# Kernel tuning notes

Hardware: AMD Instinct MI355X
Metric: run time of the kernel (lower is better)

Reference implementation:

```python
import jax, jax.numpy as jnp
import numpy as np

N_NODES = 10000
N_EDGES = 160000
IN_F = 512
H_F = 512
OUT_F = 512


def _graph_conv(x, W, b, src, dst, norm_out, norm_in):
    # DGL GraphConv, norm='both': out = D_in^{-1/2} A D_out^{-1/2} X W + b
    xs = x * norm_out[:, None]            # scale src features by out-deg^-1/2
    msgs = xs[src]                        # gather: [E, F]
    agg = jax.ops.segment_sum(msgs, dst, num_segments=N_NODES)  # scatter-sum
    agg = agg * norm_in[:, None]          # scale by in-deg^-1/2
    return agg @ W + b


def setup_inputs() -> dict:
    key = jax.random.key(0)
    ks = jax.random.split(key, 10)
    inputs = jax.random.normal(ks[0], (N_NODES, IN_F), dtype=jnp.float32)
    src = jax.random.randint(ks[1], (N_EDGES,), 0, N_NODES, dtype=jnp.int32)
    dst = jax.random.randint(ks[2], (N_EDGES,), 0, N_NODES, dtype=jnp.int32)
    # Glorot-ish init for GraphConv weights, zero bias (DGL default)
    def glorot(k, fan_in, fan_out):
        s = jnp.sqrt(6.0 / (fan_in + fan_out)).astype(jnp.float32)
        return jax.random.uniform(k, (fan_in, fan_out), jnp.float32, -s, s)
    W1 = glorot(ks[3], IN_F, H_F)
    b1 = jnp.zeros((H_F,), jnp.float32)
    W2 = glorot(ks[4], H_F, H_F)
    b2 = jnp.zeros((H_F,), jnp.float32)
    W3 = glorot(ks[5], H_F, OUT_F)
    b3 = jnp.zeros((OUT_F,), jnp.float32)
    return {"inputs": inputs, "W1": W1, "b1": b1, "W2": W2, "b2": b2,
            "W3": W3, "b3": b3, "src": src, "dst": dst}


def reference(inputs, W1, b1, W2, b2, W3, b3, src, dst):
    ones = jnp.ones((N_EDGES,), jnp.float32)
    deg_out = jax.ops.segment_sum(ones, src, num_segments=N_NODES)
    deg_in = jax.ops.segment_sum(ones, dst, num_segments=N_NODES)
    norm_out = jnp.where(deg_out > 0, deg_out ** -0.5, 0.0)
    norm_in = jnp.where(deg_in > 0, deg_in ** -0.5, 0.0)

    h1 = jax.nn.relu(_graph_conv(inputs, W1, b1, src, dst, norm_out, norm_in))
    h2 = jax.nn.relu(_graph_conv(h1, W2, b2, src, dst, norm_out, norm_in))
    # NOTE: original module applies gcn_layer_2 a second time here (not layer 3)
    h3 = jax.nn.relu(_graph_conv(h2, W2, b2, src, dst, norm_out, norm_in))
    h4 = _graph_conv(h2, W3, b3, src, dst, norm_out, norm_in)
    return (h4, h3, h2)
```

## Files before the change

kernel.cpp:

```cpp
#include <hip/hip_runtime.h>

#define N_NODES 10000
#define N_EDGES 160000
#define FEAT 512
#define M_PAD 10048
#define QSTRIDE 1286144

typedef unsigned int uint32;

typedef __attribute__((ext_vector_type(8))) _Float16 half8;
typedef __attribute__((ext_vector_type(4))) float f32x4;


__device__ __forceinline__ void load_lds16(const void* g, void* l) {
    __builtin_amdgcn_global_load_lds(
        (const __attribute__((address_space(1))) void*)g,
        (__attribute__((address_space(3))) void*)l, 16, 0, 0);
}

__global__ void deg_kernel(const int* __restrict__ src, const int* __restrict__ dst,
                           int* __restrict__ deg_out, int* __restrict__ deg_in) {
    int e = blockIdx.x * blockDim.x + threadIdx.x;
    if (e < N_EDGES) {
        atomicAdd(&deg_out[src[e]], 1);
        atomicAdd(&deg_in[dst[e]], 1);
    }
}

__global__ void norm_kernel(const int* __restrict__ deg_out, const int* __restrict__ deg_in,
                            float* __restrict__ norm_out, float* __restrict__ norm_in) {
    int i = blockIdx.x * blockDim.x + threadIdx.x;
    if (i < N_NODES) {
        int dob = deg_out[i], dib = deg_in[i];
        norm_out[i] = dob > 0 ? rsqrtf((float)dob) : 0.f;
        norm_in[i]  = dib > 0 ? rsqrtf((float)dib) : 0.f;
    }
}

__global__ void scan_kernel(const int* __restrict__ deg_in,
                            int* __restrict__ row_ptr, int* __restrict__ cursor) {
    __shared__ int sums[256];
    const int CHUNK = 40;
    int t = threadIdx.x;
    int start = t * CHUNK;
    int s = 0;
    for (int j = 0; j < CHUNK; j++) {
        int i = start + j;
        if (i < N_NODES) s += deg_in[i];
    }
    sums[t] = s;
    __syncthreads();
    for (int off = 1; off < 256; off <<= 1) {
        int v = (t >= off) ? sums[t - off] : 0;
        __syncthreads();
        sums[t] += v;
        __syncthreads();
    }
    int run = (t > 0) ? sums[t - 1] : 0;
    for (int j = 0; j < CHUNK; j++) {
        int i = start + j;
        if (i < N_NODES) {
            row_ptr[i] = run;
            cursor[i] = run;
            run += deg_in[i];
        }
    }
    if (t == 0) row_ptr[N_NODES] = sums[255];
}

__global__ void fill_kernel(const int* __restrict__ src, const int* __restrict__ dst,
                            int* __restrict__ cursor, int* __restrict__ edge_src) {
    int e = blockIdx.x * blockDim.x + threadIdx.x;
    if (e < N_EDGES) {
        int d = dst[e];
        int pos = atomicAdd(&cursor[d], 1);
        edge_src[pos] = src[e];
    }
}

__global__ __launch_bounds__(256) void prescale_kernel(const float* __restrict__ x,
        const float* __restrict__ norm_out, _Float16* __restrict__ xs) {
    int idx = blockIdx.x * 256 + threadIdx.x;
    if (idx >= N_NODES * 64) return;
    int node = idx >> 6, f8 = idx & 63;
    float w = norm_out[node];
    const float4* p = (const float4*)&x[(size_t)node * 512 + f8 * 8];
    float4 a = p[0], b = p[1];
    half8 h;
    h[0] = (_Float16)(a.x * w); h[1] = (_Float16)(a.y * w);
    h[2] = (_Float16)(a.z * w); h[3] = (_Float16)(a.w * w);
    h[4] = (_Float16)(b.x * w); h[5] = (_Float16)(b.y * w);
    h[6] = (_Float16)(b.z * w); h[7] = (_Float16)(b.w * w);
    int q = f8 >> 4, fl8 = f8 & 15;
    *(half8*)&xs[(size_t)q * QSTRIDE + (size_t)node * 128 + fl8 * 8] = h;
}

__global__ __launch_bounds__(64) void agg_kernel(const _Float16* __restrict__ xs,
        const int* __restrict__ edge_src, const int* __restrict__ row_ptr,
        const float* __restrict__ norm_in, _Float16* __restrict__ a_t) {
    int lane = threadIdx.x;
    int d = blockIdx.x, q = blockIdx.y;
    int fl = lane & 15, g = lane >> 4;
    float acc[8] = {};
    if (d < N_NODES) {
        int beg = row_ptr[d], end = row_ptr[d + 1];
        const _Float16* xq = xs + (size_t)q * QSTRIDE + fl * 8;
        int e = beg + g;
        for (; e + 4 < end; e += 8) {
            int s0 = edge_src[e], s1 = edge_src[e + 4];
            half8 v0 = *(const half8*)&xq[(size_t)s0 * 128];
            half8 v1 = *(const half8*)&xq[(size_t)s1 * 128];
#pragma unroll
            for (int i = 0; i < 8; i++) acc[i] += (float)v0[i] + (float)v1[i];
        }
        for (; e < end; e += 4) {
            int s = edge_src[e];
            half8 v = *(const half8*)&xq[(size_t)s * 128];
#pragma unroll
            for (int i = 0; i < 8; i++) acc[i] += (float)v[i];
        }
#pragma unroll
        for (int i = 0; i < 8; i++) {
            acc[i] += __shfl_xor(acc[i], 16);
            acc[i] += __shfl_xor(acc[i], 32);
        }
        float ni = norm_in[d];
#pragma unroll
        for (int i = 0; i < 8; i++) acc[i] *= ni;
    }
    if (g == 0) {
        half8 h8;
#pragma unroll
        for (int i = 0; i < 8; i++) h8[i] = (_Float16)acc[i];
        size_t o = (size_t)(d >> 4) * 8192 + (size_t)(q * 4 + (fl >> 2)) * 512
                 + (size_t)((fl & 3) * 16 + (d & 15)) * 8;
        *(half8*)&a_t[o] = h8;
    }
}

__global__ __launch_bounds__(256) void wsplit_kernel(const float* __restrict__ W1,
        const float* __restrict__ W2, const float* __restrict__ W3,
        _Float16* __restrict__ wt) {
    const float* W = blockIdx.y == 0 ? W1 : (blockIdx.y == 1 ? W2 : W3);
    size_t mbase = (size_t)blockIdx.y * 262144;
    int chunk = blockIdx.x * 256 + threadIdx.x;
    int i = chunk & 63;
    int kb = (chunk >> 6) & 15;
    int s = chunk >> 10;
    int n = s * 16 + (i & 15);
    int k0 = kb * 32 + (i >> 4) * 8;
    half8 h8;
#pragma unroll
    for (int j = 0; j < 8; j++)
        h8[j] = (_Float16)W[(size_t)(k0 + j) * 512 + n];
    *(half8*)&wt[mbase + (size_t)chunk * 8] = h8;
}

template <bool RELU_A, bool RELU_B, bool WRITE_C, bool WRITE_XS>
__global__ __launch_bounds__(256) void mfma_gemm(
        const _Float16* __restrict__ A_t, const _Float16* __restrict__ Bt,
        const float* __restrict__ bias_a, const float* __restrict__ bias_b,
        const float* __restrict__ norm_out,
        float* __restrict__ Ca, float* __restrict__ Cb,
        _Float16* __restrict__ xs) {
    __shared__ __align__(16) _Float16 lsA[64 * 32];
    __shared__ __align__(16) _Float16 lsB[128 * 32];
    int tid = threadIdx.x;
    int w = tid >> 6, lane = tid & 63;
    int col0 = blockIdx.x * 128;
    int row0 = blockIdx.y * 64;
    int wm = w & 1, wn = w >> 1;
    int lr = lane & 15, lq = lane >> 4;

    size_t aoff = (size_t)((row0 >> 4) + w) * 8192 + lane * 8;
    size_t boff = (size_t)((col0 >> 4) + 2 * w) * 8192 + lane * 8;
    _Float16* dA  = &lsA[(w * 64 + lane) * 8];
    _Float16* dB0 = &lsB[((2 * w) * 64 + lane) * 8];
    _Float16* dB1 = &lsB[((2 * w + 1) * 64 + lane) * 8];

    f32x4 acc[2][4] = {};

    for (int kb = 0; kb < 16; kb++) {
        size_t ko = (size_t)kb * 512;
        load_lds16(A_t + aoff + ko, dA);
        load_lds16(Bt + boff + ko, dB0);
        load_lds16(Bt + boff + 8192 + ko, dB1);
        __syncthreads();

        half8 a[2], b[4];
#pragma unroll
        for (int i = 0; i < 2; i++)
            a[i] = *(const half8*)&lsA[((wm * 2 + i) * 64 + lane) * 8];
#pragma unroll
        for (int j = 0; j < 4; j++)
            b[j] = *(const half8*)&lsB[((wn * 4 + j) * 64 + lane) * 8];
#pragma unroll
        for (int i = 0; i < 2; i++)
#pragma unroll
            for (int j = 0; j < 4; j++)
                acc[i][j] = __builtin_amdgcn_mfma_f32_16x16x32_f16(a[i], b[j], acc[i][j], 0, 0, 0);
        __syncthreads();
    }

    bool sec = (col0 >= 512);
    const float* bias = sec ? bias_b : bias_a;
    float* C = sec ? Cb : Ca;
    int cb0 = sec ? col0 - 512 : col0;
    const bool relu = sec ? RELU_B : RELU_A;

#pragma unroll
    for (int i = 0; i < 2; i++)
#pragma unroll
        for (int j = 0; j < 4; j++) {
            int col = cb0 + wn * 64 + j * 16 + lr;
            float bv = bias[col];
#pragma unroll
            for (int r = 0; r < 4; r++) {
                int row = row0 + wm * 32 + i * 16 + lq * 4 + r;
                if (row < N_NODES) {
                    float v = acc[i][j][r] + bv;
                    if (relu) v = fmaxf(v, 0.f);
                    if (WRITE_C) C[(size_t)row * 512 + col] = v;
                    if (WRITE_XS) {
                        int q = col >> 7, f = col & 127;
                        xs[(size_t)q * QSTRIDE + (size_t)row * 128 + f] =
                            (_Float16)(v * norm_out[row]);
                    }
                }
            }
        }
}

extern "C" void kernel_launch(void* const* d_in, const int* in_sizes, int n_in,
                              void* d_out, int out_size, void* d_ws, size_t ws_size,
                              hipStream_t stream) {
    const float* x  = (const float*)d_in[0];
    const float* W1 = (const float*)d_in[1];
    const float* b1 = (const float*)d_in[2];
    const float* W2 = (const float*)d_in[3];
    const float* b2 = (const float*)d_in[4];
    const float* W3 = (const float*)d_in[5];
    const float* b3 = (const float*)d_in[6];
    const int* src  = (const int*)d_in[7];
    const int* dst  = (const int*)d_in[8];
    float* out = (float*)d_out;

    int* wsi = (int*)d_ws;
    int* deg_out  = wsi;
    int* deg_in   = wsi + 10000;
    float* norm_out = (float*)(wsi + 20000);
    float* norm_in  = (float*)(wsi + 30000);
    int* row_ptr  = wsi + 40000;
    int* cursor   = wsi + 50016;
    int* edge_src = wsi + 60016;
    _Float16* wt  = (_Float16*)(wsi + 220016);
    _Float16* a_t = wt + 786432;
    _Float16* xs  = a_t + (size_t)M_PAD * 512;

    float* h4 = out;
    float* h3 = out + 5120000;
    float* h2 = out + 10240000;

    hipMemsetAsync(d_ws, 0, 20000 * sizeof(int), stream);

    deg_kernel<<<(N_EDGES + 255) / 256, 256, 0, stream>>>(src, dst, deg_out, deg_in);
    norm_kernel<<<(N_NODES + 255) / 256, 256, 0, stream>>>(deg_out, deg_in, norm_out, norm_in);
    scan_kernel<<<1, 256, 0, stream>>>(deg_in, row_ptr, cursor);
    fill_kernel<<<(N_EDGES + 255) / 256, 256, 0, stream>>>(src, dst, cursor, edge_src);
    wsplit_kernel<<<dim3(128, 3), 256, 0, stream>>>(W1, W2, W3, wt);
    prescale_kernel<<<(N_NODES * 64 + 255) / 256, 256, 0, stream>>>(x, norm_out, xs);

    _Float16* wt1 = wt;
    _Float16* wt2 = wt + 262144;

    dim3 ga(M_PAD, 4);
    dim3 g1(4, M_PAD / 64);
    dim3 g2(8, M_PAD / 64);

    agg_kernel<<<ga, 64, 0, stream>>>(xs, edge_src, row_ptr, norm_in, a_t);
    mfma_gemm<true, true, false, true><<<g1, 256, 0, stream>>>(
        a_t, wt1, b1, b1, norm_out, h2, h2, xs);
    agg_kernel<<<ga, 64, 0, stream>>>(xs, edge_src, row_ptr, norm_in, a_t);
    mfma_gemm<true, true, true, true><<<g1, 256, 0, stream>>>(
        a_t, wt2, b2, b2, norm_out, h2, h2, xs);
    agg_kernel<<<ga, 64, 0, stream>>>(xs, edge_src, row_ptr, norm_in, a_t);
    mfma_gemm<true, false, true, false><<<g2, 256, 0, stream>>>(
        a_t, wt2, b2, b3, norm_out, h3, h4, xs);
}
```

Before: 289.9 us.

## Fuse graph setup into one cooperative kernel and unroll aggregation to four edges

Replaces the memset and six small setup kernels (degree count, norm, scan, CSR fill, weight conversion, prescale) with a single cooperative-launch kernel that separates phases with grid-wide syncs. This is meant to remove per-launch overhead and idle gaps between tiny kernels. Separately, the aggregation inner loop now processes four gathered edges per iteration instead of two, giving more memory-level parallelism. Risks are the cost of grid.sync, a 1024-block cooperative grid that must be co-resident, the scan running on one block while the others compute norms, and higher register pressure in agg.

```diff
diff --git a/kernel.cpp b/kernel.cpp
--- a/kernel.cpp
+++ b/kernel.cpp
@@ -1,4 +1,7 @@
 #include <hip/hip_runtime.h>
+#include <hip/hip_cooperative_groups.h>
+
+namespace cg = cooperative_groups;
 
 #define N_NODES 10000
 #define N_EDGES 160000
@@ -18,81 +21,102 @@
         (__attribute__((address_space(3))) void*)l, 16, 0, 0);
 }
 
-__global__ void deg_kernel(const int* __restrict__ src, const int* __restrict__ dst,
-                           int* __restrict__ deg_out, int* __restrict__ deg_in) {
-    int e = blockIdx.x * blockDim.x + threadIdx.x;
-    if (e < N_EDGES) {
+__global__ __launch_bounds__(256) void setup_kernel(
+        const int* __restrict__ src, const int* __restrict__ dst,
+        const float* __restrict__ W1, const float* __restrict__ W2,
+        const float* __restrict__ W3, const float* __restrict__ x,
+        int* __restrict__ deg_out, int* __restrict__ deg_in,
+        float* __restrict__ norm_out, float* __restrict__ norm_in,
+        int* __restrict__ row_ptr, int* __restrict__ cursor,
+        int* __restrict__ edge_src, _Float16* __restrict__ wt,
+        _Float16* __restrict__ xs) {
+    cg::grid_group grid = cg::this_grid();
+    __shared__ int sums[256];
+    const int tid = blockIdx.x * 256 + threadIdx.x;
+    const int nth = gridDim.x * 256;
+
+    for (int i = tid; i < N_NODES; i += nth) { deg_out[i] = 0; deg_in[i] = 0; }
+    for (int c = tid; c < 3 * 32768; c += nth) {
+        int m = c >> 15, chunk = c & 32767;
+        const float* W = m == 0 ? W1 : (m == 1 ? W2 : W3);
+        int i = chunk & 63;
+        int kb = (chunk >> 6) & 15;
+        int s = chunk >> 10;
+        int n = s * 16 + (i & 15);
+        int k0 = kb * 32 + (i >> 4) * 8;
+        half8 h8;
+#pragma unroll
+        for (int j = 0; j < 8; j++)
+            h8[j] = (_Float16)W[(size_t)(k0 + j) * 512 + n];
+        *(half8*)&wt[(size_t)m * 262144 + (size_t)chunk * 8] = h8;
+    }
+    __threadfence();
+    grid.sync();
+
+    for (int e = tid; e < N_EDGES; e += nth) {
         atomicAdd(&deg_out[src[e]], 1);
         atomicAdd(&deg_in[dst[e]], 1);
     }
-}
-
-__global__ void norm_kernel(const int* __restrict__ deg_out, const int* __restrict__ deg_in,
-                            float* __restrict__ norm_out, float* __restrict__ norm_in) {
-    int i = blockIdx.x * blockDim.x + threadIdx.x;
-    if (i < N_NODES) {
-        int dob = deg_out[i], dib = deg_in[i];
-        norm_out[i] = dob > 0 ? rsqrtf((float)dob) : 0.f;
-        norm_in[i]  = dib > 0 ? rsqrtf((float)dib) : 0.f;
-    }
-}
-
-__global__ void scan_kernel(const int* __restrict__ deg_in,
-                            int* __restrict__ row_ptr, int* __restrict__ cursor) {
-    __shared__ int sums[256];
-    const int CHUNK = 40;
-    int t = threadIdx.x;
-    int start = t * CHUNK;
-    int s = 0;
-    for (int j = 0; j < CHUNK; j++) {
-        int i = start + j;
-        if (i < N_NODES) s += deg_in[i];
-    }
-    sums[t] = s;
-    __syncthreads();
-    for (int off = 1; off < 256; off <<= 1) {
-        int v = (t >= off) ? sums[t - off] : 0;
+    __threadfence();
+    grid.sync();
+
+    if (blockIdx.x == 0) {
+        const int CHUNK = 40;
+        int t = threadIdx.x;
+        int start = t * CHUNK;
+        int s = 0;
+        for (int j = 0; j < CHUNK; j++) {
+            int i = start + j;
+            if (i < N_NODES) s += deg_in[i];
+        }
+        sums[t] = s;
         __syncthreads();
-        sums[t] += v;
-        __syncthreads();
-    }
-    int run = (t > 0) ? sums[t - 1] : 0;
-    for (int j = 0; j < CHUNK; j++) {
-        int i = start + j;
-        if (i < N_NODES) {
-            row_ptr[i] = run;
-            cursor[i] = run;
-            run += deg_in[i];
-        }
-    }
-    if (t == 0) row_ptr[N_NODES] = sums[255];
-}
-
-__global__ void fill_kernel(const int* __restrict__ src, const int* __restrict__ dst,
-                            int* __restrict__ cursor, int* __restrict__ edge_src) {
-    int e = blockIdx.x * blockDim.x + threadIdx.x;
-    if (e < N_EDGES) {
+        for (int off = 1; off < 256; off <<= 1) {
+            int v = (t >= off) ? sums[t - off] : 0;
+            __syncthreads();
+            sums[t] += v;
+            __syncthreads();
+        }
+        int run = (t > 0) ? sums[t - 1] : 0;
+        for (int j = 0; j < CHUNK; j++) {
+            int i = start + j;
+            if (i < N_NODES) {
+                row_ptr[i] = run;
+                cursor[i] = run;
+                run += deg_in[i];
+            }
+        }
+        if (t == 0) row_ptr[N_NODES] = sums[255];
+    } else {
+        int t2 = (blockIdx.x - 1) * 256 + threadIdx.x;
+        int n2 = (gridDim.x - 1) * 256;
+        for (int i = t2; i < N_NODES; i += n2) {
+            int dob = deg_out[i], dib = deg_in[i];
+            norm_out[i] = dob > 0 ? rsqrtf((float)dob) : 0.f;
+            norm_in[i]  = dib > 0 ? rsqrtf((float)dib) : 0.f;
+        }
+    }
+    __threadfence();
+    grid.sync();
+
+    for (int e = tid; e < N_EDGES; e += nth) {
         int d = dst[e];
         int pos = atomicAdd(&cursor[d], 1);
         edge_src[pos] = src[e];
     }
-}
-
-__global__ __launch_bounds__(256) void prescale_kernel(const float* __restrict__ x,
-        const float* __restrict__ norm_out, _Float16* __restrict__ xs) {
-    int idx = blockIdx.x * 256 + threadIdx.x;
-    if (idx >= N_NODES * 64) return;
-    int node = idx >> 6, f8 = idx & 63;
-    float w = norm_out[node];
-    const float4* p = (const float4*)&x[(size_t)node * 512 + f8 * 8];
-    float4 a = p[0], b = p[1];
-    half8 h;
-    h[0] = (_Float16)(a.x * w); h[1] = (_Float16)(a.y * w);
-    h[2] = (_Float16)(a.z * w); h[3] = (_Float16)(a.w * w);
-    h[4] = (_Float16)(b.x * w); h[5] = (_Float16)(b.y * w);
-    h[6] = (_Float16)(b.z * w); h[7] = (_Float16)(b.w * w);
-    int q = f8 >> 4, fl8 = f8 & 15;
-    *(half8*)&xs[(size_t)q * QSTRIDE + (size_t)node * 128 + fl8 * 8] = h;
+    for (int idx = tid; idx < N_NODES * 64; idx += nth) {
+        int node = idx >> 6, f8 = idx & 63;
+        float w = norm_out[node];
+        const float4* p = (const float4*)&x[(size_t)node * 512 + f8 * 8];
+        float4 a = p[0], b = p[1];
+        half8 h;
+        h[0] = (_Float16)(a.x * w); h[1] = (_Float16)(a.y * w);
+        h[2] = (_Float16)(a.z * w); h[3] = (_Float16)(a.w * w);
+        h[4] = (_Float16)(b.x * w); h[5] = (_Float16)(b.y * w);
+        h[6] = (_Float16)(b.z * w); h[7] = (_Float16)(b.w * w);
+        int q = f8 >> 4, fl8 = f8 & 15;
+        *(half8*)&xs[(size_t)q * QSTRIDE + (size_t)node * 128 + fl8 * 8] = h;
+    }
 }
 
 __global__ __launch_bounds__(64) void agg_kernel(const _Float16* __restrict__ xs,
@@ -106,12 +130,16 @@
         int beg = row_ptr[d], end = row_ptr[d + 1];
         const _Float16* xq = xs + (size_t)q * QSTRIDE + fl * 8;
         int e = beg + g;
-        for (; e + 4 < end; e += 8) {
+        for (; e + 12 < end; e += 16) {
             int s0 = edge_src[e], s1 = edge_src[e + 4];
+            int s2 = edge_src[e + 8], s3 = edge_src[e + 12];
             half8 v0 = *(const half8*)&xq[(size_t)s0 * 128];
             half8 v1 = *(const half8*)&xq[(size_t)s1 * 128];
-#pragma unroll
-            for (int i = 0; i < 8; i++) acc[i] += (float)v0[i] + (float)v1[i];
+            half8 v2 = *(const half8*)&xq[(size_t)s2 * 128];
+            half8 v3 = *(const half8*)&xq[(size_t)s3 * 128];
+#pragma unroll
+            for (int i = 0; i < 8; i++)
+                acc[i] += ((float)v0[i] + (float)v1[i]) + ((float)v2[i] + (float)v3[i]);
         }
         for (; e < end; e += 4) {
             int s = edge_src[e];
@@ -136,24 +164,6 @@
                  + (size_t)((fl & 3) * 16 + (d & 15)) * 8;
         *(half8*)&a_t[o] = h8;
     }
-}
-
-__global__ __launch_bounds__(256) void wsplit_kernel(const float* __restrict__ W1,
-        const float* __restrict__ W2, const float* __restrict__ W3,
-        _Float16* __restrict__ wt) {
-    const float* W = blockIdx.y == 0 ? W1 : (blockIdx.y == 1 ? W2 : W3);
-    size_t mbase = (size_t)blockIdx.y * 262144;
-    int chunk = blockIdx.x * 256 + threadIdx.x;
-    int i = chunk & 63;
-    int kb = (chunk >> 6) & 15;
-    int s = chunk >> 10;
-    int n = s * 16 + (i & 15);
-    int k0 = kb * 32 + (i >> 4) * 8;
-    half8 h8;
-#pragma unroll
-    for (int j = 0; j < 8; j++)
-        h8[j] = (_Float16)W[(size_t)(k0 + j) * 512 + n];
-    *(half8*)&wt[mbase + (size_t)chunk * 8] = h8;
 }
 
 template <bool RELU_A, bool RELU_B, bool WRITE_C, bool WRITE_XS>
@@ -261,14 +271,12 @@
     float* h3 = out + 5120000;
     float* h2 = out + 10240000;
 
-    hipMemsetAsync(d_ws, 0, 20000 * sizeof(int), stream);
-
-    deg_kernel<<<(N_EDGES + 255) / 256, 256, 0, stream>>>(src, dst, deg_out, deg_in);
-    norm_kernel<<<(N_NODES + 255) / 256, 256, 0, stream>>>(deg_out, deg_in, norm_out, norm_in);
-    scan_kernel<<<1, 256, 0, stream>>>(deg_in, row_ptr, cursor);
-    fill_kernel<<<(N_EDGES + 255) / 256, 256, 0, stream>>>(src, dst, cursor, edge_src);
-    wsplit_kernel<<<dim3(128, 3), 256, 0, stream>>>(W1, W2, W3, wt);
-    prescale_kernel<<<(N_NODES * 64 + 255) / 256, 256, 0, stream>>>(x, norm_out, xs);
+    void* sargs[] = {(void*)&src, (void*)&dst, (void*)&W1, (void*)&W2, (void*)&W3,
+                     (void*)&x, (void*)&deg_out, (void*)&deg_in, (void*)&norm_out,
+                     (void*)&norm_in, (void*)&row_ptr, (void*)&cursor,
+                     (void*)&edge_src, (void*)&wt, (void*)&xs};
+    hipLaunchCooperativeKernel(reinterpret_cast<void*>(setup_kernel),
+                               dim3(1024), dim3(256), sargs, 0, stream);
 
     _Float16* wt1 = wt;
     _Float16* wt2 = wt + 262144;
```

New measurement: 743.2 us. 2.56x slower.
